# Optimization experiments

Hardware: AMD Instinct MI355X
Metric: run time of the kernel (lower is better)

The kernel has to match this reference:

```python
import jax, jax.numpy as jnp
import numpy as np

B, L, D = 2, 2048, 2048
H, KVH, HD = 16, 4, 128
GROUPS = H // KVH  # 4 == KVH (required by this module's v_proj sizing)
EPS = 1e-6
SCALE = HD ** -0.5
NEG = -1e9


def setup_inputs() -> dict:
    key = jax.random.key(0)
    ks = jax.random.split(key, 6)
    hidden_states = jax.random.normal(ks[0], (B, L, D), jnp.float32)
    # RoPE tables (b, l, head_dim), HF-style: angles duplicated across halves
    half = HD // 2
    inv_freq = 1.0 / (1e6 ** (jnp.arange(half, dtype=jnp.float32) / half))
    ang = jnp.arange(L, dtype=jnp.float32)[:, None] * inv_freq[None, :]  # (L, half)
    emb = jnp.concatenate([ang, ang], axis=-1)  # (L, HD)
    cos = jnp.broadcast_to(jnp.cos(emb)[None], (B, L, HD))
    sin = jnp.broadcast_to(jnp.sin(emb)[None], (B, L, HD))
    # additive causal mask (b,1,l,l)
    m = jnp.triu(jnp.full((L, L), NEG, jnp.float32), k=1)
    attention_mask = jnp.broadcast_to(m[None, None], (B, 1, L, L))
    s = 0.02
    wq = jax.random.normal(ks[1], (H * HD, D), jnp.float32) * s
    wk = jax.random.normal(ks[2], (KVH * HD, D), jnp.float32) * s
    wv = jax.random.normal(ks[3], (KVH * HD, D), jnp.float32) * s
    wo = jax.random.normal(ks[4], (D, H * HD), jnp.float32) * s
    q_norm_w = jnp.ones((HD,), jnp.float32)
    k_norm_w = jnp.ones((HD,), jnp.float32)
    return dict(hidden_states=hidden_states, cos=cos, sin=sin,
                attention_mask=attention_mask, wq=wq, wk=wk, wv=wv, wo=wo,
                q_norm_w=q_norm_w, k_norm_w=k_norm_w)


def _rmsnorm(x, w):
    var = jnp.mean(x * x, axis=-1, keepdims=True)
    return w * (x * jax.lax.rsqrt(var + EPS))


def _rotate_half(x):
    u, v = jnp.split(x, 2, axis=-1)
    return jnp.concatenate([-v, u], axis=-1)


def reference(hidden_states, cos, sin, attention_mask, wq, wk, wv, wo, q_norm_w, k_norm_w):
    b, l, _ = hidden_states.shape
    q = (hidden_states @ wq.T).reshape(b, l, H, HD).transpose(0, 2, 1, 3)   # (b,H,l,hd)
    k = (hidden_states @ wk.T).reshape(b, l, KVH, HD).transpose(0, 2, 1, 3)
    v = (hidden_states @ wv.T).reshape(b, l, KVH, HD).transpose(0, 2, 1, 3)
    q = _rmsnorm(q, q_norm_w)
    k = _rmsnorm(k, k_norm_w)
    c = cos[:, None]  # (b,1,l,hd)
    s = sin[:, None]
    q = q * c + _rotate_half(q) * s
    k = k * c + _rotate_half(k) * s
    # GQA: repeat each kv head GROUPS times consecutively (matches repeat_n)
    k = jnp.repeat(k, GROUPS, axis=1)
    v = jnp.repeat(v, GROUPS, axis=1)
    attn = jnp.einsum('bhqd,bhkd->bhqk', q, k) * SCALE + attention_mask
    attn = jax.nn.softmax(attn, axis=-1)
    out = jnp.einsum('bhqk,bhkd->bhqd', attn, v)
    out = out.transpose(0, 2, 1, 3).reshape(b, l, H * HD)
    return out @ wo.T
```

## Files before the change

### kernel.cpp

```cpp
#include <hip/hip_runtime.h>


#define SEQL 2048
#define DMODEL 2048
#define NH 16
#define NKVH 4
#define HDIM 128
#define SCALE_QK 0.08838834764831845f
#define LOG2E 1.4426950408889634f
#define INFF 3.0e38f

typedef __attribute__((ext_vector_type(8))) short bf16x8;
typedef __attribute__((ext_vector_type(4))) float f32x4;
typedef __attribute__((ext_vector_type(4))) unsigned int u32x4;

__device__ __forceinline__ unsigned short f2bf(float x) {
  union { float f; unsigned u; } v; v.f = x;
  unsigned r = v.u + 0x7fffu + ((v.u >> 16) & 1u);
  return (unsigned short)(r >> 16);
}
__device__ __forceinline__ float bf2f(unsigned short u) {
  union { unsigned u; float f; } v; v.u = ((unsigned)u) << 16;
  return v.f;
}

__global__ __launch_bounds__(256) void cast_kernel(const float* __restrict__ src,
                                                   unsigned short* __restrict__ dst,
                                                   int n8) {
  int i = blockIdx.x * 256 + threadIdx.x;
  if (i >= n8) return;
  const f32x4* s4 = (const f32x4*)src;
  f32x4 a = s4[2 * i], b = s4[2 * i + 1];
  union { unsigned short s[8]; u32x4 v; } o;
  o.s[0] = f2bf(a[0]); o.s[1] = f2bf(a[1]); o.s[2] = f2bf(a[2]); o.s[3] = f2bf(a[3]);
  o.s[4] = f2bf(b[0]); o.s[5] = f2bf(b[1]); o.s[6] = f2bf(b[2]); o.s[7] = f2bf(b[3]);
  ((u32x4*)dst)[i] = o.v;
}

__global__ __launch_bounds__(256) void cast3_kernel(const float* __restrict__ s0,
                                                    const float* __restrict__ s1,
                                                    const float* __restrict__ s2,
                                                    unsigned short* __restrict__ dst,
                                                    int n0, int n1, int n2) {
  int i = blockIdx.x * 256 + threadIdx.x;
  const float* src;
  int j;
  if (i < n0) { src = s0; j = i; }
  else if (i < n0 + n1) { src = s1; j = i - n0; }
  else if (i < n0 + n1 + n2) { src = s2; j = i - n0 - n1; }
  else return;
  const f32x4* s4 = (const f32x4*)src;
  f32x4 a = s4[2 * j], b = s4[2 * j + 1];
  union { unsigned short s[8]; u32x4 v; } o;
  o.s[0] = f2bf(a[0]); o.s[1] = f2bf(a[1]); o.s[2] = f2bf(a[2]); o.s[3] = f2bf(a[3]);
  o.s[4] = f2bf(b[0]); o.s[5] = f2bf(b[1]); o.s[6] = f2bf(b[2]); o.s[7] = f2bf(b[3]);
  ((u32x4*)dst)[i] = o.v;
}

template <int OUT_BF16>
__global__ __launch_bounds__(256) void gemm_bt(const unsigned short* __restrict__ A,
                                               const unsigned short* __restrict__ B,
                                               void* __restrict__ C,
                                               int M, int N, int K) {
  __shared__ unsigned short As[128 * 64];
  __shared__ unsigned short Bs[128 * 64];
  int tid = threadIdx.x;
  int w = tid >> 6, lane = tid & 63;
  int lr = lane & 15, lg = lane >> 4;
  int m0 = blockIdx.y * 128, n0 = blockIdx.x * 128;
  int wr = (w >> 1) * 64, wc = (w & 1) * 64;
  f32x4 zero4 = {0.f, 0.f, 0.f, 0.f};
  f32x4 acc[4][4];
  for (int i = 0; i < 4; ++i)
    for (int j = 0; j < 4; ++j) acc[i][j] = zero4;

  for (int k0 = 0; k0 < K; k0 += 64) {
    __syncthreads();
    for (int i = 0; i < 4; ++i) {
      int o = i * 4096 + w * 1024 + lane * 16;
      int row = o >> 7, cb = o & 127;
      int scb = cb ^ ((row & 7) << 4);
      const char* ga = (const char*)(A + (size_t)(m0 + row) * K + k0) + scb;
      const char* gb = (const char*)(B + (size_t)(n0 + row) * K + k0) + scb;
      __builtin_amdgcn_global_load_lds(
          (const __attribute__((address_space(1))) void*)ga,
          (__attribute__((address_space(3))) void*)((char*)As + i * 4096 + w * 1024),
          16, 0, 0);
      __builtin_amdgcn_global_load_lds(
          (const __attribute__((address_space(1))) void*)gb,
          (__attribute__((address_space(3))) void*)((char*)Bs + i * 4096 + w * 1024),
          16, 0, 0);
    }
    asm volatile("s_waitcnt vmcnt(0)" ::: "memory");
    __syncthreads();

    for (int kk = 0; kk < 2; ++kk) {
      bf16x8 a[4], b[4];
      for (int i = 0; i < 4; ++i) {
        int row = wr + i * 16 + lr;
        int col = kk * 64 + lg * 16;
        a[i] = *(const bf16x8*)((const char*)As + row * 128 + (col ^ ((row & 7) << 4)));
      }
      for (int j = 0; j < 4; ++j) {
        int row = wc + j * 16 + lr;
        int col = kk * 64 + lg * 16;
        b[j] = *(const bf16x8*)((const char*)Bs + row * 128 + (col ^ ((row & 7) << 4)));
      }
      for (int i = 0; i < 4; ++i)
        for (int j = 0; j < 4; ++j)
          acc[i][j] = __builtin_amdgcn_mfma_f32_16x16x32_bf16(a[i], b[j], acc[i][j], 0, 0, 0);
    }
  }

  for (int i = 0; i < 4; ++i)
    for (int j = 0; j < 4; ++j) {
      int row = m0 + wr + i * 16 + lg * 4;
      int col = n0 + wc + j * 16 + lr;
      for (int r = 0; r < 4; ++r) {
        if (OUT_BF16)
          ((unsigned short*)C)[(size_t)(row + r) * N + col] = f2bf(acc[i][j][r]);
        else
          ((float*)C)[(size_t)(row + r) * N + col] = acc[i][j][r];
      }
    }
}

__global__ __launch_bounds__(64) void prep_kernel(const unsigned short* __restrict__ qkv,
                                                  const float* __restrict__ cosb,
                                                  const float* __restrict__ sinb,
                                                  const float* __restrict__ qw,
                                                  const float* __restrict__ kw,
                                                  unsigned short* __restrict__ Qb,
                                                  unsigned short* __restrict__ Kb,
                                                  unsigned short* __restrict__ Vtb)
{
  int l = blockIdx.x, b = blockIdx.y, d = threadIdx.x;
  size_t row = (size_t)b * SEQL + l;
  const unsigned short* src = qkv + row * 3072;
  float c0 = cosb[row * HDIM + d], c1 = cosb[row * HDIM + d + 64];
  float s0 = sinb[row * HDIM + d], s1 = sinb[row * HDIM + d + 64];
  float qw0 = qw[d], qw1 = qw[d + 64];
  float kw0 = kw[d], kw1 = kw[d + 64];
  const float qscale = SCALE_QK * LOG2E;

  float x0[20], x1[20], ss[20];
#pragma unroll
  for (int h = 0; h < 20; ++h) {
    x0[h] = bf2f(src[h * HDIM + d]);
    x1[h] = bf2f(src[h * HDIM + d + 64]);
    ss[h] = x0[h] * x0[h] + x1[h] * x1[h];
  }
#pragma unroll
  for (int m = 1; m < 64; m <<= 1) {
#pragma unroll
    for (int h = 0; h < 20; ++h) ss[h] += __shfl_xor(ss[h], m);
  }
#pragma unroll
  for (int h = 0; h < 16; ++h) {
    float inv = rsqrtf(ss[h] * (1.0f / 128.0f) + 1e-6f);
    float n0 = x0[h] * inv * qw0, n1 = x1[h] * inv * qw1;
    float r0 = (n0 * c0 - n1 * s0) * qscale;
    float r1 = (n1 * c1 + n0 * s1) * qscale;
    unsigned short* dst = Qb + (((size_t)(b * NH + h)) * SEQL + l) * HDIM;
    dst[d] = f2bf(r0);
    dst[d + 64] = f2bf(r1);
  }
#pragma unroll
  for (int h = 0; h < 4; ++h) {
    float inv = rsqrtf(ss[16 + h] * (1.0f / 128.0f) + 1e-6f);
    float n0 = x0[16 + h] * inv * kw0, n1 = x1[16 + h] * inv * kw1;
    float r0 = n0 * c0 - n1 * s0;
    float r1 = n1 * c1 + n0 * s1;
    unsigned short* dst = Kb + (((size_t)(b * NKVH + h)) * SEQL + l) * HDIM;
    dst[d] = f2bf(r0);
    dst[d + 64] = f2bf(r1);
  }
#pragma unroll
  for (int h = 0; h < NKVH; ++h) {
    unsigned short v0 = src[2560 + h * HDIM + d];
    unsigned short v1 = src[2560 + h * HDIM + d + 64];
    unsigned short* dst = Vtb + ((size_t)(b * NKVH + h) * HDIM) * SEQL;
    dst[(size_t)d * SEQL + l] = v0;
    dst[(size_t)(d + 64) * SEQL + l] = v1;
  }
}

__global__ __launch_bounds__(512) void flash_kernel(const unsigned short* __restrict__ Qb,
                                                    const unsigned short* __restrict__ Kb,
                                                    const unsigned short* __restrict__ Vtb,
                                                    unsigned short* __restrict__ AOb)
{
  __shared__ unsigned short Ks[2][64 * 128];
  __shared__ unsigned short Vs[2][128 * 64];
  __shared__ unsigned short Ps[128 * 64];

  int tid = threadIdx.x, w = tid >> 6, lane = tid & 63;
  int lr = lane & 15, lg = lane >> 4;
  int bh = blockIdx.y;
  int qt = (bh < 16) ? (int)blockIdx.x : 15 - (int)blockIdx.x;
  int b = bh >> 4, h = bh & 15, hk = h >> 2;
  int q0 = qt * 128;
  int qrow_base = 16 * w + lg * 4;

  const unsigned short* Qg =
      Qb + (((size_t)(b * NH + h)) * SEQL + q0 + 16 * w + lr) * HDIM + lg * 8;
  bf16x8 aq[4];
  for (int kk = 0; kk < 4; ++kk) aq[kk] = *(const bf16x8*)(Qg + kk * 32);

  const unsigned short* Kg0 = Kb + ((size_t)(b * NKVH + hk)) * SEQL * HDIM;
  const unsigned short* Vg0 = Vtb + ((size_t)(b * NKVH + hk)) * HDIM * SEQL;

  float m_run[4], l_part[4];
  f32x4 zero4 = {0.f, 0.f, 0.f, 0.f};
  f32x4 o_acc[8];
  for (int r = 0; r < 4; ++r) { m_run[r] = -INFF; l_part[r] = 0.f; }
  for (int f = 0; f < 8; ++f) o_acc[f] = zero4;

  int nt = 2 * qt + 2;

  u32x4 kr[2], vr[2];

  auto load_tile = [&](int tt) {
    int k0n = tt * 64;
    for (int i = 0; i < 2; ++i) {
      int o = i * 8192 + tid * 16;
      kr[i] = *(const u32x4*)((const char*)Kg0 + (size_t)(k0n + (o >> 8)) * 256 + (o & 255));
      vr[i] = *(const u32x4*)((const char*)Vg0 +
                              (size_t)(o >> 7) * (SEQL * 2) + (size_t)k0n * 2 + (o & 127));
    }
  };
  auto stage_tile = [&](char* kb, char* vb) {
    for (int i = 0; i < 2; ++i) {
      int o = i * 8192 + tid * 16;
      int krow = o >> 8;
      *(u32x4*)(kb + (o ^ ((krow & 7) << 4))) = kr[i];
      int vrow = o >> 7;
      *(u32x4*)(vb + (o ^ ((vrow & 7) << 4))) = vr[i];
    }
  };
  auto compute_tile = [&](int t, const char* kb, const char* vb) {
    int k0 = t * 64;
    if (k0 > q0 + 16 * w + 15) return;
    bool needmask = (k0 + 63 > q0 + 16 * w);

    f32x4 s[4];
    for (int j = 0; j < 4; ++j) s[j] = zero4;
    __builtin_amdgcn_s_setprio(1);
    for (int kk = 0; kk < 4; ++kk)
      for (int j = 0; j < 4; ++j) {
        int row = j * 16 + lr;
        bf16x8 bk = *(const bf16x8*)(kb +
                     ((row * 256 + kk * 64 + lg * 16) ^ ((lr & 7) << 4)));
        s[j] = __builtin_amdgcn_mfma_f32_16x16x32_bf16(aq[kk], bk, s[j], 0, 0, 0);
      }
    __builtin_amdgcn_s_setprio(0);

    for (int r = 0; r < 4; ++r) {
      int qrow = qrow_base + r;
      float v[4];
      if (needmask) {
        int qg = q0 + qrow;
        for (int j = 0; j < 4; ++j)
          v[j] = (k0 + j * 16 + lr <= qg) ? s[j][r] : -INFF;
      } else {
        for (int j = 0; j < 4; ++j) v[j] = s[j][r];
      }
      float mxl = fmaxf(fmaxf(v[0], v[1]), fmaxf(v[2], v[3]));
      if (!__all(mxl <= m_run[r] + 8.f)) {
        float mx = mxl;
        mx = fmaxf(mx, __shfl_xor(mx, 1));
        mx = fmaxf(mx, __shfl_xor(mx, 2));
        mx = fmaxf(mx, __shfl_xor(mx, 4));
        mx = fmaxf(mx, __shfl_xor(mx, 8));
        float m_new = fmaxf(m_run[r], mx);
        float sc = __builtin_amdgcn_exp2f(m_run[r] - m_new);
        l_part[r] *= sc;
        for (int f = 0; f < 8; ++f) o_acc[f][r] *= sc;
        m_run[r] = m_new;
      }
      float m_use = m_run[r];
      float rs = 0.f;
      for (int j = 0; j < 4; ++j) {
        float p = __builtin_amdgcn_exp2f(v[j] - m_use);
        rs += p;
        *(unsigned short*)((char*)Ps +
            ((qrow * 128 + (j * 16 + lr) * 2) ^ ((qrow & 7) << 4))) = f2bf(p);
      }
      l_part[r] += rs;
    }

    __builtin_amdgcn_s_setprio(1);
    for (int kk = 0; kk < 2; ++kk) {
      int prow = 16 * w + lr;
      bf16x8 ap = *(const bf16x8*)((const char*)Ps +
                   ((prow * 128 + kk * 64 + lg * 16) ^ ((lr & 7) << 4)));
      for (int f = 0; f < 8; ++f) {
        int vrow = f * 16 + lr;
        bf16x8 bv = *(const bf16x8*)(vb +
                     ((vrow * 128 + kk * 64 + lg * 16) ^ ((lr & 7) << 4)));
        o_acc[f] = __builtin_amdgcn_mfma_f32_16x16x32_bf16(ap, bv, o_acc[f], 0, 0, 0);
      }
    }
    __builtin_amdgcn_s_setprio(0);
  };

  load_tile(0);
  stage_tile((char*)Ks[0], (char*)Vs[0]);
  if (nt > 1) load_tile(1);
  asm volatile("s_waitcnt lgkmcnt(0)" ::: "memory");
  __builtin_amdgcn_s_barrier();
  __builtin_amdgcn_sched_barrier(0);

  for (int t = 0; t < nt; t += 2) {
    if (t + 1 < nt) stage_tile((char*)Ks[1], (char*)Vs[1]);
    if (t + 2 < nt) load_tile(t + 2);
    compute_tile(t, (const char*)Ks[0], (const char*)Vs[0]);
    asm volatile("s_waitcnt lgkmcnt(0)" ::: "memory");
    __builtin_amdgcn_s_barrier();
    __builtin_amdgcn_sched_barrier(0);
    if (t + 1 >= nt) break;
    if (t + 2 < nt) stage_tile((char*)Ks[0], (char*)Vs[0]);
    if (t + 3 < nt) load_tile(t + 3);
    compute_tile(t + 1, (const char*)Ks[1], (const char*)Vs[1]);
    asm volatile("s_waitcnt lgkmcnt(0)" ::: "memory");
    __builtin_amdgcn_s_barrier();
    __builtin_amdgcn_sched_barrier(0);
  }

  unsigned short* dst = AOb + ((size_t)b * SEQL + q0) * DMODEL + h * HDIM;
  for (int r = 0; r < 4; ++r) {
    float l = l_part[r];
    l += __shfl_xor(l, 1);
    l += __shfl_xor(l, 2);
    l += __shfl_xor(l, 4);
    l += __shfl_xor(l, 8);
    float inv = 1.0f / l;
    for (int f = 0; f < 8; ++f)
      dst[(size_t)(qrow_base + r) * DMODEL + f * 16 + lr] = f2bf(o_acc[f][r] * inv);
  }
}

extern "C" void kernel_launch(void* const* d_in, const int* in_sizes, int n_in,
                              void* d_out, int out_size, void* d_ws, size_t ws_size,
                              hipStream_t stream) {
  const float* hidden = (const float*)d_in[0];
  const float* cosb = (const float*)d_in[1];
  const float* sinb = (const float*)d_in[2];
  const float* wq = (const float*)d_in[4];
  const float* wk = (const float*)d_in[5];
  const float* wv = (const float*)d_in[6];
  const float* wo = (const float*)d_in[7];
  const float* qw = (const float*)d_in[8];
  const float* kw = (const float*)d_in[9];
  float* out = (float*)d_out;

  char* ws = (char*)d_ws;
  unsigned short* Xb    = (unsigned short*)(ws + 0);
  unsigned short* Wqkvb = (unsigned short*)(ws + 16777216);
  unsigned short* QKVb  = (unsigned short*)(ws + 29360128);
  unsigned short* Qbuf  = (unsigned short*)(ws + 54525952);
  unsigned short* Kbuf  = (unsigned short*)(ws + 71303168);
  unsigned short* Vtb   = (unsigned short*)(ws + 75497472);
  unsigned short* AOb   = Xb;
  unsigned short* Wob   = QKVb;

  cast_kernel<<<(8388608 / 8 + 255) / 256, 256, 0, stream>>>(hidden, Xb, 8388608 / 8);
  cast3_kernel<<<(786432 + 255) / 256, 256, 0, stream>>>(wq, wk, wv, Wqkvb,
                                                         524288, 131072, 131072);

  gemm_bt<1><<<dim3(3072 / 128, 4096 / 128), 256, 0, stream>>>(Xb, Wqkvb, QKVb, 4096, 3072, 2048);

  prep_kernel<<<dim3(SEQL, 2), 64, 0, stream>>>(QKVb, cosb, sinb, qw, kw, Qbuf, Kbuf, Vtb);

  cast_kernel<<<(4194304 / 8 + 255) / 256, 256, 0, stream>>>(wo, Wob, 4194304 / 8);

  flash_kernel<<<dim3(SEQL / 128, 2 * NH), 512, 0, stream>>>(Qbuf, Kbuf, Vtb, AOb);

  gemm_bt<0><<<dim3(2048 / 128, 4096 / 128), 256, 0, stream>>>(AOb, Wob, out, 4096, 2048, 2048);
}
```

Baseline: 235.4 us.

## Double-buffer LDS tiles in projection GEMM to overlap global loads with MFMA

Splits the GEMM's shared-memory A/B tiles into two buffers. The next k-tile is now issued via global_load_lds while MFMAs run on the current one, with one wait and barrier per tile instead of two. This hides global-memory latency behind compute. The cost is doubled LDS use (64KB per block), which may reduce occupancy, plus fully unrolled inner loops that raise register pressure.

```diff
diff --git a/kernel.cpp b/kernel.cpp
--- a/kernel.cpp
+++ b/kernel.cpp
@@ -62,8 +62,8 @@
                                                const unsigned short* __restrict__ B,
                                                void* __restrict__ C,
                                                int M, int N, int K) {
-  __shared__ unsigned short As[128 * 64];
-  __shared__ unsigned short Bs[128 * 64];
+  __shared__ unsigned short As[2][128 * 64];
+  __shared__ unsigned short Bs[2][128 * 64];
   int tid = threadIdx.x;
   int w = tid >> 6, lane = tid & 63;
   int lr = lane & 15, lg = lane >> 4;
@@ -74,8 +74,8 @@
   for (int i = 0; i < 4; ++i)
     for (int j = 0; j < 4; ++j) acc[i][j] = zero4;
 
-  for (int k0 = 0; k0 < K; k0 += 64) {
-    __syncthreads();
+  auto stage = [&](int buf, int k0) {
+#pragma unroll
     for (int i = 0; i < 4; ++i) {
       int o = i * 4096 + w * 1024 + lane * 16;
       int row = o >> 7, cb = o & 127;
@@ -84,32 +84,56 @@
       const char* gb = (const char*)(B + (size_t)(n0 + row) * K + k0) + scb;
       __builtin_amdgcn_global_load_lds(
           (const __attribute__((address_space(1))) void*)ga,
-          (__attribute__((address_space(3))) void*)((char*)As + i * 4096 + w * 1024),
+          (__attribute__((address_space(3))) void*)((char*)As[buf] + o),
           16, 0, 0);
       __builtin_amdgcn_global_load_lds(
           (const __attribute__((address_space(1))) void*)gb,
-          (__attribute__((address_space(3))) void*)((char*)Bs + i * 4096 + w * 1024),
+          (__attribute__((address_space(3))) void*)((char*)Bs[buf] + o),
           16, 0, 0);
     }
-    asm volatile("s_waitcnt vmcnt(0)" ::: "memory");
-    __syncthreads();
-
+  };
+  auto compute = [&](const char* as, const char* bs) {
+#pragma unroll
     for (int kk = 0; kk < 2; ++kk) {
       bf16x8 a[4], b[4];
+#pragma unroll
       for (int i = 0; i < 4; ++i) {
         int row = wr + i * 16 + lr;
         int col = kk * 64 + lg * 16;
-        a[i] = *(const bf16x8*)((const char*)As + row * 128 + (col ^ ((row & 7) << 4)));
-      }
+        a[i] = *(const bf16x8*)(as + row * 128 + (col ^ ((row & 7) << 4)));
+      }
+#pragma unroll
       for (int j = 0; j < 4; ++j) {
         int row = wc + j * 16 + lr;
         int col = kk * 64 + lg * 16;
-        b[j] = *(const bf16x8*)((const char*)Bs + row * 128 + (col ^ ((row & 7) << 4)));
-      }
+        b[j] = *(const bf16x8*)(bs + row * 128 + (col ^ ((row & 7) << 4)));
+      }
+#pragma unroll
       for (int i = 0; i < 4; ++i)
+#pragma unroll
         for (int j = 0; j < 4; ++j)
           acc[i][j] = __builtin_amdgcn_mfma_f32_16x16x32_bf16(a[i], b[j], acc[i][j], 0, 0, 0);
     }
+  };
+
+  int nkt = K >> 6;
+  stage(0, 0);
+  asm volatile("s_waitcnt vmcnt(0)" ::: "memory");
+  __builtin_amdgcn_s_barrier();
+  __builtin_amdgcn_sched_barrier(0);
+
+  for (int kt = 0; kt < nkt; kt += 2) {
+    if (kt + 1 < nkt) stage(1, (kt + 1) << 6);
+    compute((const char*)As[0], (const char*)Bs[0]);
+    asm volatile("s_waitcnt vmcnt(0) lgkmcnt(0)" ::: "memory");
+    __builtin_amdgcn_s_barrier();
+    __builtin_amdgcn_sched_barrier(0);
+    if (kt + 1 >= nkt) break;
+    if (kt + 2 < nkt) stage(0, (kt + 2) << 6);
+    compute((const char*)As[1], (const char*)Bs[1]);
+    asm volatile("s_waitcnt vmcnt(0) lgkmcnt(0)" ::: "memory");
+    __builtin_amdgcn_s_barrier();
+    __builtin_amdgcn_sched_barrier(0);
   }
 
   for (int i = 0; i < 4; ++i)
```

Result: slower. 272.2 us (+15.7%).
